# Performance work log

Measured on AMD Instinct MI355X. Metric: run time of the kernel, lower is better.

The kernel has to match this reference:

```python
import jax, jax.numpy as jnp
import numpy as np
from jax.ops import segment_sum, segment_max

ALPHA = 0.01  # leaky relu slope

def _cmul(a, b):
    # complex multiply on last-axis (re, im) pairs
    re = a[..., 0] * b[..., 0] - a[..., 1] * b[..., 1]
    im = a[..., 0] * b[..., 1] + a[..., 1] * b[..., 0]
    return jnp.stack((re, im), axis=-1)

def setup_inputs() -> dict:
    key = jax.random.key(0)
    ks = jax.random.split(key, 8)
    N, D, M, E, L, H, R, FH = 50000, 64, 3, 100000, 4, 8, 5, 128
    return {
        "features": jax.random.normal(ks[0], (N, D), jnp.float32),
        "attn1_w": jax.random.normal(ks[1], (M, H, D), jnp.float32) * 0.1,
        "attn2":   jax.random.normal(ks[2], (M, H, D), jnp.float32) * 0.1,
        "r_vec":   jax.random.normal(ks[3], (R, D // 2, 2), jnp.float32),
        "proj_w1": jax.random.normal(ks[4], (FH, H * D), jnp.float32) * 0.05,
        "proj_b1": jnp.zeros((FH,), jnp.float32),
        "proj_w2": jax.random.normal(ks[5], (1, FH), jnp.float32) * 0.1,
        "inst":    jax.random.randint(ks[6], (M, E, L), 0, N),
        "etypes":  jax.random.randint(ks[7], (M, L - 1), 0, 2 * R, dtype=jnp.int32),
    }

def reference(features, attn1_w, attn2, r_vec, proj_w1, proj_b1, proj_w2, inst, etypes):
    N, D = features.shape
    M, E, L = inst.shape
    H = attn1_w.shape[1]
    # --- conjugate-augmented, L2-normalized relation rotations ([2R, D/2, 2]) ---
    rn = r_vec / jnp.linalg.norm(r_vec, axis=2, keepdims=True)
    conj = rn * jnp.array([1.0, -1.0], rn.dtype)
    r_full = jnp.stack((rn, conj), axis=1).reshape(2 * r_vec.shape[0], r_vec.shape[1], 2)

    node_embs = []  # per-metapath [N, H*D]
    for m in range(M):
        # SemanticEncoder: gather + rotation recurrence + mean over path positions
        edata = features[inst[m]]                       # [E, L, D]
        edc = edata.reshape(E, L, D // 2, 2)
        # final_r_vec: backward cumulative complex product; position L-1 = identity
        ident = jnp.concatenate(
            [jnp.ones((D // 2, 1), edata.dtype), jnp.zeros((D // 2, 1), edata.dtype)], axis=-1)
        fr = [None] * L
        fr[L - 1] = ident
        for i in range(L - 2, -1, -1):
            fr[i] = _cmul(fr[i + 1], r_full[etypes[m, i]])
        fr = jnp.stack(fr, axis=0)                      # [L, D/2, 2]
        rotated = _cmul(edc, fr[None])                  # [E, L, D/2, 2] (pos L-1 rotated by identity)
        me = rotated.reshape(E, L, D).mean(axis=1)      # metapath embedding [E, D]

        # MessageAggregator: GAT-style segment softmax over instances per dst node
        dst = inst[m, :, 0]                             # [E]
        a1 = features[dst] @ attn1_w[m].T               # [E, H]
        a2 = jnp.einsum('ed,hd->eh', me, attn2[m])      # [E, H]
        a = jax.nn.leaky_relu(a1 + a2, ALPHA)           # [E, H]
        amax = segment_max(a, dst, num_segments=N)      # [N, H]
        amax = jnp.where(jnp.isfinite(amax), amax, 0.0)
        ex = jnp.exp(a - amax[dst])                     # [E, H]
        den = segment_sum(ex, dst, num_segments=N)      # [N, H]
        attn = ex / jnp.where(den[dst] > 0, den[dst], 1.0)
        agg = segment_sum(attn[:, :, None] * me[:, None, :], dst, num_segments=N)  # [N, H, D]
        node_embs.append(jax.nn.elu(agg).reshape(N, H * D))

    # Subgraph_Fusion: semantic attention over metapaths
    z = jnp.stack(node_embs, axis=1)                    # [N, M, H*D]
    w = jnp.tanh(z @ proj_w1.T + proj_b1) @ proj_w2.T   # [N, M, 1]
    beta = jax.nn.softmax(w.mean(axis=0), axis=0)       # [M, 1]
    out = (beta[None] * z).sum(axis=1)                  # [N, H*D]
    return out
```

## Files before the change

### kernel.cpp

```cpp
#include <hip/hip_runtime.h>
#include <hip/hip_bf16.h>
#include <hip/hip_fp16.h>
#include <math.h>

#define NN 50000
#define DD 64
#define MM 3
#define EE 100000
#define LL 4
#define HH 8
#define FHH 128
#define HD 512
#define NROWS (NN*MM)
#define LRELU_ALPHA 0.01f

#define WSUM_BINS 256
#define WSUM_SZ (MM*WSUM_BINS)
#define BINS (MM*NN)
#define NBLK ((BINS + 1023)/1024)
#define GT_TILE 224

#define FCVT_B 3125
#define CW1_B  64
#define UGEN_B 3
#define HISTG  392
#define HIST_B (HISTG*MM)
#define PREP_B (FCVT_B + CW1_B + UGEN_B + HIST_B + 1)

#define GT_B   (224*MM)
#define MID_B  (GT_B + NBLK)

#define SCAT_B (HISTG*MM)
#define SEGC_B ((BINS + 255)/256)
#define SCT_B  (SCAT_B + SEGC_B)

#define OFF_ZB    0
#define OFF_WSUM  (NROWS*HD/2)
#define OFF_BETA  (OFF_WSUM + WSUM_SZ)
#define OFF_W1BF  (OFF_BETA + 16)
#define OFF_WU    (OFF_W1BF + 32768)
#define OFF_FRS   (OFF_WU + 6144)
#define OFF_GT    (OFF_FRS + 768)
#define OFF_INTS  (OFF_GT + MM*NN*32)
#define IOFF_CNT    0
#define IOFF_CURSOR (IOFF_CNT + BINS)
#define IOFF_PART   (IOFF_CURSOR + BINS)
#define IOFF_BSUM   (IOFF_PART + BINS)
#define IOFF_BTOP   (IOFF_BSUM + 256)
#define IOFF_SEG8   (IOFF_BTOP + 256)
#define IOFF_REC    (IOFF_SEG8 + 8*BINS)
#define INTS_END    (IOFF_REC + 4*MM*EE)
#define OFF_F16   (OFF_INTS + INTS_END)

typedef short v8s __attribute__((ext_vector_type(8)));
typedef float v4f __attribute__((ext_vector_type(4)));

__device__ __forceinline__ float elu_f(float x) {
    return x > 0.f ? x : (__expf(x) - 1.f);
}

__device__ __forceinline__ float tanh_fast(float x) {
    float e = __expf(2.f * x);
    return 1.f - 2.f / (e + 1.f);
}

__device__ __forceinline__ unsigned int pk_bf16x2(float x, float y) {
    float2 f2; f2.x = x; f2.y = y;
    __hip_bfloat162 h = __float22bfloat162_rn(f2);
    union { __hip_bfloat162 h; unsigned int u; } cv;
    cv.h = h;
    return cv.u;
}

__device__ __forceinline__ unsigned int pk_h2(float x, float y) {
    __half2 h = __floats2half2_rn(x, y);
    union { __half2 h; unsigned int u; } cv;
    cv.h = h;
    return cv.u;
}

__device__ __forceinline__ float bf_lo(unsigned int u) {
    union { unsigned int x; float f; } c; c.x = u << 16; return c.f;
}
__device__ __forceinline__ float bf_hi(unsigned int u) {
    union { unsigned int x; float f; } c; c.x = u & 0xffff0000u; return c.f;
}

__device__ __forceinline__ __half2 u2h(unsigned int u) {
    union { unsigned int x; __half2 h; } c; c.x = u; return c.h;
}
__device__ __forceinline__ unsigned int h2u(__half2 h) {
    union { __half2 h; unsigned int x; } c; c.h = h; return c.x;
}

__device__ __forceinline__ unsigned int pk_fma(unsigned int x, unsigned int c, unsigned int a) {
    unsigned int d;
    asm("v_pk_fma_f16 %0, %1, %2, %3"
        : "=v"(d) : "v"(x), "v"(c), "v"(a));
    return d;
}
__device__ __forceinline__ unsigned int pk_fma_swap0(unsigned int x, unsigned int c, unsigned int a) {
    unsigned int d;
    asm("v_pk_fma_f16 %0, %1, %2, %3 op_sel:[1,0,0] op_sel_hi:[0,1,1]"
        : "=v"(d) : "v"(x), "v"(c), "v"(a));
    return d;
}
__device__ __forceinline__ unsigned int pk_fma_bcast0(unsigned int x, unsigned int c, unsigned int a) {
    unsigned int d;
    asm("v_pk_fma_f16 %0, %1, %2, %3 op_sel:[0,0,0] op_sel_hi:[0,1,1]"
        : "=v"(d) : "v"(x), "v"(c), "v"(a));
    return d;
}
__device__ __forceinline__ unsigned int pk_fma_bcast0hi(unsigned int x, unsigned int c, unsigned int a) {
    unsigned int d;
    asm("v_pk_fma_f16 %0, %1, %2, %3 op_sel:[1,0,0] op_sel_hi:[1,1,1]"
        : "=v"(d) : "v"(x), "v"(c), "v"(a));
    return d;
}

__device__ __forceinline__ void build_frs(
    float frs[LL][DD/2][2], const float* r_vec, const int* etypes, int m, int t)
{
    if (t < DD/2) {
        float cr = 1.f, ci = 0.f;
        frs[LL-1][t][0] = 1.f; frs[LL-1][t][1] = 0.f;
        for (int i = LL-2; i >= 0; --i) {
            int et = etypes[m*(LL-1) + i];
            float rr = r_vec[((et>>1)*(DD/2) + t)*2 + 0];
            float ri = r_vec[((et>>1)*(DD/2) + t)*2 + 1];
            float inv = rsqrtf(rr*rr + ri*ri);
            rr *= inv; ri *= inv;
            if (et & 1) ri = -ri;
            float nr = cr*rr - ci*ri;
            float ni = cr*ri + ci*rr;
            cr = nr; ci = ni;
            frs[i][t][0] = cr; frs[i][t][1] = ci;
        }
    }
}

__global__ __launch_bounds__(256) void prep_kernel(
    const float* __restrict__ features, ushort* __restrict__ f16,
    const float* __restrict__ w1, ushort* __restrict__ w1bf,
    const float* __restrict__ r_vec, const int* __restrict__ etypes,
    const float* __restrict__ attn1_w, const float* __restrict__ attn2,
    float* __restrict__ Wu, unsigned int* __restrict__ frs_h,
    const int* __restrict__ inst, int* __restrict__ cnt,
    float* __restrict__ wsum)
{
    const int b = blockIdx.x;
    const int t = threadIdx.x;
    if (b < FCVT_B) {
        int i = b*256 + t;
        float4 v = ((const float4*)features)[i];
        ((uint2*)f16)[i] = make_uint2(pk_h2(v.x, v.y), pk_h2(v.z, v.w));
    } else if (b < FCVT_B + CW1_B) {
        int i = (b - FCVT_B)*256 + t;
        float4 v = ((const float4*)w1)[i];
        uint2 p; p.x = pk_bf16x2(v.x, v.y); p.y = pk_bf16x2(v.z, v.w);
        ((uint2*)w1bf)[i] = p;
    } else if (b < FCVT_B + CW1_B + UGEN_B) {
        const int m = b - (FCVT_B + CW1_B);
        __shared__ float frs[LL][DD/2][2];
        build_frs(frs, r_vec, etypes, m, t);
        __syncthreads();
        if (t < 32) {
            unsigned int vals[8];
            #pragma unroll
            for (int l = 0; l < LL; ++l) {
                float fr = 0.25f * frs[l][t][0];
                float fi = 0.25f * frs[l][t][1];
                vals[2*l+0] = pk_h2(fr, fr);
                vals[2*l+1] = pk_h2(-fi, fi);
            }
            uint4* dst = (uint4*)frs_h + (m*32 + t)*2;
            dst[0] = make_uint4(vals[0], vals[1], vals[2], vals[3]);
            dst[1] = make_uint4(vals[4], vals[5], vals[6], vals[7]);
        }
        for (int idx = t; idx < 32*64; idx += 256) {
            int j = idx >> 6, d = idx & 63, p = d >> 1;
            int l = (j < 8) ? 0 : (j >> 3);
            int h = j & 7;
            float fr = frs[l][p][0], fi = frs[l][p][1];
            float w2r = attn2[m*HD + h*DD + 2*p];
            float w2i = attn2[m*HD + h*DD + 2*p + 1];
            float u = (d & 1) ? (fr*w2i - fi*w2r) : (fr*w2r + fi*w2i);
            float val = 0.25f * u + ((j < 8) ? attn1_w[m*HD + h*DD + d] : 0.f);
            Wu[(m*32 + j)*64 + d] = val;
        }
    } else if (b < FCVT_B + CW1_B + UGEN_B + HIST_B) {
        int idx = b - (FCVT_B + CW1_B + UGEN_B);
        int m = idx / HISTG;
        int e = (idx - m*HISTG)*256 + t;
        if (e < EE) {
            int dst = inst[((size_t)m*EE + e)*LL];
            atomicAdd(&cnt[m*NN + dst], 1);
        }
    } else {
        for (int i = t; i < WSUM_SZ; i += 256) wsum[i] = 0.f;
    }
}

__global__ __launch_bounds__(256) void mid_kernel(
    const float* __restrict__ features,
    const float* __restrict__ Wu,
    ushort* __restrict__ gt16,
    const int* __restrict__ cnt,
    int* __restrict__ part, int* __restrict__ bsum)
{
    __shared__ float xs[GT_TILE*65];
    __shared__ int sd[256];
    const int b = blockIdx.x;
    const int t = threadIdx.x;
    if (b < GT_B) {
        const int m = b / 224;
        const int node0 = (b - m*224) * GT_TILE;
        #pragma unroll
        for (int i = 0; i < 14; ++i) {
            int idx = t + 256*i;
            int r = idx >> 4, c4 = idx & 15;
            int gr = node0 + r;
            float4 v = make_float4(0.f,0.f,0.f,0.f);
            if (gr < NN) v = ((const float4*)features)[gr*16 + c4];
            float* dst = &xs[r*65 + c4*4];
            dst[0]=v.x; dst[1]=v.y; dst[2]=v.z; dst[3]=v.w;
        }
        __syncthreads();
        if (t >= GT_TILE) return;
        int node = node0 + t;
        float acc[32];
        #pragma unroll
        for (int j=0;j<32;++j) acc[j]=0.f;
        const float* Wm = Wu + m*2048;
        for (int d = 0; d < 64; ++d) {
            float x = xs[t*65 + d];
            #pragma unroll
            for (int j = 0; j < 32; ++j)
                acc[j] += x * Wm[j*64 + d];
        }
        if (node < NN) {
            ushort* o = gt16 + ((size_t)m*NN + node)*32;
            #pragma unroll
            for (int j4 = 0; j4 < 8; ++j4) {
                uint2 p;
                p.x = pk_h2(acc[j4*4+0], acc[j4*4+1]);
                p.y = pk_h2(acc[j4*4+2], acc[j4*4+3]);
                ((uint2*)o)[j4] = p;
            }
        }
    } else {
        const int bb = b - GT_B;
        const int base = bb*1024 + t*4;
        int v0=0,v1=0,v2=0,v3=0;
        if (base+3 < BINS) {
            int4 v = *(const int4*)&cnt[base];
            v0=v.x; v1=v.y; v2=v.z; v3=v.w;
        } else {
            if (base+0 < BINS) v0 = cnt[base+0];
            if (base+1 < BINS) v1 = cnt[base+1];
            if (base+2 < BINS) v2 = cnt[base+2];
            if (base+3 < BINS) v3 = cnt[base+3];
        }
        int tot = v0+v1+v2+v3;
        sd[t] = tot; __syncthreads();
        #pragma unroll
        for (int off = 1; off < 256; off <<= 1) {
            int val = (t >= off) ? sd[t-off] : 0;
            __syncthreads();
            sd[t] += val;
            __syncthreads();
        }
        int excl = sd[t] - tot;
        if (base+0 < BINS) part[base+0] = excl;
        if (base+1 < BINS) part[base+1] = excl + v0;
        if (base+2 < BINS) part[base+2] = excl + v0 + v1;
        if (base+3 < BINS) part[base+3] = excl + v0 + v1 + v2;
        if (t == 255) bsum[bb] = sd[255];
    }
}

__global__ __launch_bounds__(256) void scan_tops_kernel(
    const int* __restrict__ bsum, int* __restrict__ btop)
{
    __shared__ int sd[256];
    const int t = threadIdx.x;
    int v = (t < NBLK) ? bsum[t] : 0;
    sd[t] = v; __syncthreads();
    #pragma unroll
    for (int off = 1; off < 256; off <<= 1) {
        int val = (t >= off) ? sd[t-off] : 0;
        __syncthreads();
        sd[t] += val;
        __syncthreads();
    }
    if (t < NBLK) btop[t] = sd[t] - v;
}

__global__ __launch_bounds__(256) void scat_kernel(
    const int4* __restrict__ inst4, const int* __restrict__ part,
    const int* __restrict__ btop, int* __restrict__ cursor,
    int4* __restrict__ rec, const int* __restrict__ cnt,
    int* __restrict__ seg8)
{
    const int b = blockIdx.x;
    const int t = threadIdx.x;
    if (b < SCAT_B) {
        int m = b / HISTG;
        int e = (b - m*HISTG)*256 + t;
        if (e >= EE) return;
        int4 v = inst4[(size_t)m*EE + e];
        int bin = m*NN + v.x;
        int c = atomicAdd(&cursor[bin], 1);
        int pos = part[bin] + btop[bin >> 10] + c;
        rec[pos] = make_int4(v.y, v.z, v.w, 0);
        if (c < 2) {
            int* s = seg8 + bin*8 + 2 + c*3;
            s[0] = v.y; s[1] = v.z; s[2] = v.w;
        }
    } else {
        int i = (b - SCAT_B)*256 + t;
        if (i < BINS)
            ((int2*)seg8)[i*4] = make_int2(part[i] + btop[i >> 10], cnt[i]);
    }
}

__global__ __launch_bounds__(128) void node_kernel(
    const unsigned int* __restrict__ f16u,
    const unsigned int* __restrict__ frs_h,
    const int4*  __restrict__ rec4,
    const int*   __restrict__ seg8,
    const ushort* __restrict__ gt16,
    ushort* __restrict__ Zb)
{
    const int m = blockIdx.y;
    const int t = threadIdx.x;
    const int lane = t & 63;
    const int hl   = lane & 31;
    const int half = lane >> 5;
    const int wid  = t >> 6;
    const int node = blockIdx.x*2 + wid;

    const int bin = m*NN + node;
    ushort* zrow = Zb + ((size_t)node*MM + m)*HD;
    const int4 sa = ((const int4*)seg8)[bin*2 + 0];
    const int4 sb = ((const int4*)seg8)[bin*2 + 1];

    const uint4* fh = (const uint4*)frs_h + ((size_t)(m*32 + hl))*2;
    const uint4 ca = fh[0], cb = fh[1];
    const unsigned int ux0 = f16u[(size_t)node*32 + hl];
    const float c0 = __half2float(((const __half*)gt16)[(size_t)bin*32 + (hl & 7)]);

    const int start = __builtin_amdgcn_readfirstlane(sa.x);
    const int ecnt  = __builtin_amdgcn_readfirstlane(sa.y);
    if (ecnt == 0) {
        ((uint4*)zrow)[lane] = make_uint4(0u,0u,0u,0u);
        return;
    }

    int4 rpre = make_int4(0,0,0,0);
    if (ecnt > 2) {
        int myq = 2 + half;
        int qq = (myq < ecnt) ? myq : (ecnt - 1);
        rpre = rec4[start + qq];
    }

    unsigned int me0u = h2u(__hmul2(u2h(ux0), u2h(ca.x)));
    me0u = pk_fma_swap0(ux0, ca.y, me0u);

    const int lsel = hl >> 3;
    const bool gm = (hl >= 8);
    const __half* gtmh = (const __half*)gt16 + (size_t)m*NN*32;

    unsigned int acc[HH];
    #pragma unroll
    for (int h = 0; h < HH; ++h) acc[h] = 0u;
    float den = 0.f;

    auto edge = [&](int i1, int i2, int i3, bool valid) {
        int idxg = (lsel == 1) ? i1 : ((lsel == 2) ? i2 : i3);
        float gv = 0.f;
        if (gm) gv = __half2float(gtmh[(size_t)idxg*32 + hl]);
        unsigned int u1 = f16u[(size_t)i1*32 + hl];
        unsigned int u2 = f16u[(size_t)i2*32 + hl];
        unsigned int u3 = f16u[(size_t)i3*32 + hl];
        gv += __shfl_xor(gv, 16);
        gv += __shfl_xor(gv, 8);
        unsigned int me = me0u;
        me = pk_fma(u1, ca.z, me);
        me = pk_fma_swap0(u1, ca.w, me);
        me = pk_fma(u2, cb.x, me);
        me = pk_fma_swap0(u2, cb.y, me);
        me = pk_fma(u3, cb.z, me);
        me = pk_fma_swap0(u3, cb.w, me);
        float a = c0 + gv;
        a = fmaxf(a, LRELU_ALPHA*a);
        float ex = valid ? __expf(a) : 0.f;
        den += ex;
        float exn = __shfl_xor(ex, 1);
        unsigned int ex2 = pk_h2(ex, exn);
        #pragma unroll
        for (int j = 0; j < 4; ++j) {
            unsigned int eu = __shfl(ex2, (lane & 32) + 2*j);
            acc[2*j]   = pk_fma_bcast0  (eu, me, acc[2*j]);
            acc[2*j+1] = pk_fma_bcast0hi(eu, me, acc[2*j+1]);
        }
    };

    {
        bool useB = (half == 1) && (ecnt >= 2);
        int i1 = useB ? sb.y : sa.z;
        int i2 = useB ? sb.z : sa.w;
        int i3 = useB ? sb.w : sb.x;
        edge(i1, i2, i3, half == 0 || ecnt >= 2);
    }
    if (ecnt > 2) {
        edge(rpre.x, rpre.y, rpre.z, (2 + half) < ecnt);
        for (int q = 4; q < ecnt; q += 2) {
            int myq = q + half;
            bool valid = (myq < ecnt);
            int qq = valid ? myq : (ecnt - 1);
            int4 r = rec4[start + qq];
            edge(r.x, r.y, r.z, valid);
        }
    }

    #pragma unroll
    for (int h = 0; h < HH; ++h) {
        unsigned int au = __shfl_xor(acc[h], 32);
        acc[h] = h2u(__hadd2(u2h(acc[h]), u2h(au)));
    }
    den += __shfl_xor(den, 32);

    const int hbase = half ? 4 : 0;
    #pragma unroll
    for (int hh = 0; hh < 4; ++hh) {
        int h = hbase + hh;
        unsigned int sel = half ? acc[hh+4] : acc[hh];
        float dh = __shfl(den, h);
        float inv = __builtin_amdgcn_rcpf(dh);
        float2 v = __half22float2(u2h(sel));
        float vr = elu_f(v.x * inv);
        float vi = elu_f(v.y * inv);
        ((unsigned int*)zrow)[h*32 + hl] = pk_bf16x2(vr, vi);
    }
}


__global__ __launch_bounds__(256,3) void wproj_kernel(
    const ushort* __restrict__ Zb,
    const ushort* __restrict__ w1bf,
    const float* __restrict__ b1,
    const float* __restrict__ w2,
    float* __restrict__ wsum)
{
    __shared__ ushort As[128*72];
    __shared__ ushort Bs[128*72];
    __shared__ float wacc[MM];
    const int t = threadIdx.x;
    const int row0 = blockIdx.x * 128;
    if (t < MM) wacc[t] = 0.f;
    const int lane = t & 63;
    const int wid  = t >> 6;
    const int ln   = lane & 15;
    const int quad = lane >> 4;
    const int wr   = wid >> 1;
    const int wc   = wid & 1;

    v4f acc[4][4];
    #pragma unroll
    for (int i=0;i<4;++i)
        #pragma unroll
        for (int j=0;j<4;++j)
            acc[i][j] = (v4f){0.f,0.f,0.f,0.f};

    const uint4* zb4 = (const uint4*)Zb;
    const uint4* wb4 = (const uint4*)w1bf;

    for (int kt = 0; kt < 8; ++kt) {
        __syncthreads();
        #pragma unroll
        for (int i = 0; i < 4; ++i) {
            int idx = t + 256*i;
            int r = idx >> 3, k8 = idx & 7;
            int gr = row0 + r;
            uint4 v = make_uint4(0u,0u,0u,0u);
            if (gr < NROWS) v = zb4[(size_t)gr*64 + kt*8 + k8];
            *(uint4*)&As[r*72 + k8*8] = v;
        }
        #pragma unroll
        for (int i = 0; i < 4; ++i) {
            int idx = t + 256*i;
            int f = idx >> 3, k8 = idx & 7;
            uint4 v = wb4[f*64 + kt*8 + k8];
            *(uint4*)&Bs[f*72 + k8*8] = v;
        }
        __syncthreads();
        #pragma unroll
        for (int kk = 0; kk < 2; ++kk) {
            v8s a[4], b[4];
            #pragma unroll
            for (int i=0;i<4;++i)
                a[i] = *(const v8s*)&As[(wr*64 + i*16 + ln)*72 + kk*32 + quad*8];
            #pragma unroll
            for (int j=0;j<4;++j)
                b[j] = *(const v8s*)&Bs[(wc*64 + j*16 + ln)*72 + kk*32 + quad*8];
            #pragma unroll
            for (int i=0;i<4;++i)
                #pragma unroll
                for (int j=0;j<4;++j)
                    acc[i][j] = __builtin_amdgcn_mfma_f32_16x16x32_bf16(
                        a[i], b[j], acc[i][j], 0, 0, 0);
        }
    }

    float b1v[4], w2v[4];
    #pragma unroll
    for (int j=0;j<4;++j) {
        int col = wc*64 + j*16 + ln;
        b1v[j] = b1[col];
        w2v[j] = w2[col];
    }
    #pragma unroll
    for (int i=0;i<4;++i) {
        #pragma unroll
        for (int reg=0;reg<4;++reg) {
            float s = 0.f;
            #pragma unroll
            for (int j=0;j<4;++j)
                s += tanh_fast(acc[i][j][reg] + b1v[j]) * w2v[j];
            s += __shfl_xor(s, 1);
            s += __shfl_xor(s, 2);
            s += __shfl_xor(s, 4);
            s += __shfl_xor(s, 8);
            int grow = row0 + wr*64 + i*16 + quad*4 + reg;
            if (ln == 0 && grow < NROWS)
                atomicAdd(&wacc[grow % MM], s);
        }
    }
    __syncthreads();
    if (t < MM)
        atomicAdd(&wsum[t*WSUM_BINS + (blockIdx.x & (WSUM_BINS-1))], wacc[t]);
}

__global__ void beta_kernel(const float* __restrict__ wsum, float* __restrict__ beta)
{
    __shared__ float sm[MM];
    int t = threadIdx.x;
    if (t < MM) {
        float s = 0.f;
        for (int i = 0; i < WSUM_BINS; ++i) s += wsum[t*WSUM_BINS + i];
        sm[t] = s / (float)NN;
    }
    __syncthreads();
    if (t < MM) {
        float a = sm[0], b = sm[1], c = sm[2];
        float mx = fmaxf(a, fmaxf(b, c));
        float e0 = __expf(a-mx), e1 = __expf(b-mx), e2 = __expf(c-mx);
        float tot = e0+e1+e2;
        float mine = (t==0?e0:(t==1?e1:e2));
        beta[t] = mine/tot;
    }
}

__global__ __launch_bounds__(256) void out_kernel(
    const ushort* __restrict__ Zb, const float* __restrict__ beta,
    float* __restrict__ out)
{
    int i = blockIdx.x*256 + threadIdx.x;
    int n  = i >> 6;
    int jj = i & 63;
    float b0 = beta[0], b1v = beta[1], b2 = beta[2];
    const uint4* zb4 = (const uint4*)Zb;
    uint4 v0 = zb4[((size_t)n*MM + 0)*64 + jj];
    uint4 v1 = zb4[((size_t)n*MM + 1)*64 + jj];
    uint4 v2 = zb4[((size_t)n*MM + 2)*64 + jj];
    float o[8];
    o[0] = b0*bf_lo(v0.x) + b1v*bf_lo(v1.x) + b2*bf_lo(v2.x);
    o[1] = b0*bf_hi(v0.x) + b1v*bf_hi(v1.x) + b2*bf_hi(v2.x);
    o[2] = b0*bf_lo(v0.y) + b1v*bf_lo(v1.y) + b2*bf_lo(v2.y);
    o[3] = b0*bf_hi(v0.y) + b1v*bf_hi(v1.y) + b2*bf_hi(v2.y);
    o[4] = b0*bf_lo(v0.z) + b1v*bf_lo(v1.z) + b2*bf_lo(v2.z);
    o[5] = b0*bf_hi(v0.z) + b1v*bf_hi(v1.z) + b2*bf_hi(v2.z);
    o[6] = b0*bf_lo(v0.w) + b1v*bf_lo(v1.w) + b2*bf_lo(v2.w);
    o[7] = b0*bf_hi(v0.w) + b1v*bf_hi(v1.w) + b2*bf_hi(v2.w);
    float4* op = (float4*)(out + (size_t)n*HD + jj*8);
    op[0] = make_float4(o[0],o[1],o[2],o[3]);
    op[1] = make_float4(o[4],o[5],o[6],o[7]);
}

extern "C" void kernel_launch(void* const* d_in, const int* in_sizes, int n_in,
                              void* d_out, int out_size, void* d_ws, size_t ws_size,
                              hipStream_t stream) {
    const float* features = (const float*)d_in[0];
    const float* attn1_w  = (const float*)d_in[1];
    const float* attn2    = (const float*)d_in[2];
    const float* r_vec    = (const float*)d_in[3];
    const float* proj_w1  = (const float*)d_in[4];
    const float* proj_b1  = (const float*)d_in[5];
    const float* proj_w2  = (const float*)d_in[6];
    const int*   inst     = (const int*)d_in[7];
    const int*   etypes   = (const int*)d_in[8];
    float* out = (float*)d_out;

    float* ws    = (float*)d_ws;
    ushort* Zb   = (ushort*)(ws + OFF_ZB);
    float* wsum  = ws + OFF_WSUM;
    float* beta  = ws + OFF_BETA;
    ushort* w1bf = (ushort*)(ws + OFF_W1BF);
    float* Wu    = ws + OFF_WU;
    unsigned int* frs_h = (unsigned int*)(ws + OFF_FRS);
    ushort* gt16 = (ushort*)(ws + OFF_GT);
    int* ints    = (int*)(ws + OFF_INTS);
    int* cnt     = ints + IOFF_CNT;
    int* cursor  = ints + IOFF_CURSOR;
    int* part    = ints + IOFF_PART;
    int* bsum    = ints + IOFF_BSUM;
    int* btop    = ints + IOFF_BTOP;
    int* seg8    = ints + IOFF_SEG8;
    int4* rec4   = (int4*)(ints + IOFF_REC);
    ushort* f16  = (ushort*)(ws + OFF_F16);

    hipMemsetAsync(cnt, 0, (size_t)2*BINS*sizeof(int), stream);

    prep_kernel<<<PREP_B, 256, 0, stream>>>(
        features, f16, proj_w1, w1bf, r_vec, etypes, attn1_w, attn2,
        Wu, frs_h, inst, cnt, wsum);
    mid_kernel<<<MID_B, 256, 0, stream>>>(features, Wu, gt16, cnt, part, bsum);
    scan_tops_kernel<<<1, 256, 0, stream>>>(bsum, btop);
    scat_kernel<<<SCT_B, 256, 0, stream>>>(
        (const int4*)inst, part, btop, cursor, rec4, cnt, seg8);
    node_kernel<<<dim3(NN/2, MM), 128, 0, stream>>>(
        (const unsigned int*)f16, frs_h, rec4, seg8, gt16, Zb);
    wproj_kernel<<<(NROWS + 127)/128, 256, 0, stream>>>(Zb, w1bf, proj_b1, proj_w2, wsum);
    beta_kernel<<<1, 64, 0, stream>>>(wsum, beta);
    out_kernel<<<NN*64/256, 256, 0, stream>>>(Zb, beta, out);
}
```

Measured before the change: 353.2 us.

## Map one node per half-wavefront in node_kernel instead of one per wavefront

Each half-wave of 32 lanes now owns a separate destination node and walks that node's edges serially, so a 64-lane wave handles two nodes. Before, the two halves split one node's edges and then merged their results with cross-half shuffles. The change removes the cross-half reduction and halves the grid, with the aim of cutting idle lanes when a node has few edges. In exchange, the loop runs to the larger of the two nodes' edge counts, so one half-wave idles through padded iterations when counts differ. It also adds a guard for a zero denominator.

Measured after the change: 344.6 us. 1.02x faster.

```diff
diff --git a/kernel.cpp b/kernel.cpp
--- a/kernel.cpp
+++ b/kernel.cpp
@@ -338,7 +338,7 @@
     const int hl   = lane & 31;
     const int half = lane >> 5;
     const int wid  = t >> 6;
-    const int node = blockIdx.x*2 + wid;
+    const int node = blockIdx.x*4 + wid*2 + half;
 
     const int bin = m*NN + node;
     ushort* zrow = Zb + ((size_t)node*MM + m)*HD;
@@ -350,18 +350,14 @@
     const unsigned int ux0 = f16u[(size_t)node*32 + hl];
     const float c0 = __half2float(((const __half*)gt16)[(size_t)bin*32 + (hl & 7)]);
 
-    const int start = __builtin_amdgcn_readfirstlane(sa.x);
-    const int ecnt  = __builtin_amdgcn_readfirstlane(sa.y);
-    if (ecnt == 0) {
-        ((uint4*)zrow)[lane] = make_uint4(0u,0u,0u,0u);
+    const int start = sa.x;
+    const int ecnt  = sa.y;
+    int eo = __shfl_xor(ecnt, 32);
+    int emax = __builtin_amdgcn_readfirstlane(max(ecnt, eo));
+    if (emax == 0) {
+        ((uint4*)zrow)[hl] = make_uint4(0u,0u,0u,0u);
+        ((uint4*)zrow)[hl + 32] = make_uint4(0u,0u,0u,0u);
         return;
-    }
-
-    int4 rpre = make_int4(0,0,0,0);
-    if (ecnt > 2) {
-        int myq = 2 + half;
-        int qq = (myq < ecnt) ? myq : (ecnt - 1);
-        rpre = rec4[start + qq];
     }
 
     unsigned int me0u = h2u(__hmul2(u2h(ux0), u2h(ca.x)));
@@ -376,7 +372,18 @@
     for (int h = 0; h < HH; ++h) acc[h] = 0u;
     float den = 0.f;
 
-    auto edge = [&](int i1, int i2, int i3, bool valid) {
+    for (int q = 0; q < emax; ++q) {
+        bool valid = (q < ecnt);
+        int i1, i2, i3;
+        if (q == 0)      { i1 = sa.z; i2 = sa.w; i3 = sb.x; }
+        else if (q == 1) { i1 = sb.y; i2 = sb.z; i3 = sb.w; }
+        else {
+            int qq = valid ? q : (ecnt > 0 ? ecnt - 1 : 0);
+            int4 r = rec4[start + qq];
+            i1 = r.x; i2 = r.y; i3 = r.z;
+        }
+        if (!valid) { i1 = node; i2 = node; i3 = node; }
+
         int idxg = (lsel == 1) ? i1 : ((lsel == 2) ? i2 : i3);
         float gv = 0.f;
         if (gm) gv = __half2float(gtmh[(size_t)idxg*32 + hl]);
@@ -404,41 +411,13 @@
             acc[2*j]   = pk_fma_bcast0  (eu, me, acc[2*j]);
             acc[2*j+1] = pk_fma_bcast0hi(eu, me, acc[2*j+1]);
         }
-    };
-
-    {
-        bool useB = (half == 1) && (ecnt >= 2);
-        int i1 = useB ? sb.y : sa.z;
-        int i2 = useB ? sb.z : sa.w;
-        int i3 = useB ? sb.w : sb.x;
-        edge(i1, i2, i3, half == 0 || ecnt >= 2);
-    }
-    if (ecnt > 2) {
-        edge(rpre.x, rpre.y, rpre.z, (2 + half) < ecnt);
-        for (int q = 4; q < ecnt; q += 2) {
-            int myq = q + half;
-            bool valid = (myq < ecnt);
-            int qq = valid ? myq : (ecnt - 1);
-            int4 r = rec4[start + qq];
-            edge(r.x, r.y, r.z, valid);
-        }
     }
 
     #pragma unroll
     for (int h = 0; h < HH; ++h) {
-        unsigned int au = __shfl_xor(acc[h], 32);
-        acc[h] = h2u(__hadd2(u2h(acc[h]), u2h(au)));
-    }
-    den += __shfl_xor(den, 32);
-
-    const int hbase = half ? 4 : 0;
-    #pragma unroll
-    for (int hh = 0; hh < 4; ++hh) {
-        int h = hbase + hh;
-        unsigned int sel = half ? acc[hh+4] : acc[hh];
-        float dh = __shfl(den, h);
-        float inv = __builtin_amdgcn_rcpf(dh);
-        float2 v = __half22float2(u2h(sel));
+        float dh = __shfl(den, (lane & 32) + h);
+        float inv = (dh > 0.f) ? __builtin_amdgcn_rcpf(dh) : 0.f;
+        float2 v = __half22float2(u2h(acc[h]));
         float vr = elu_f(v.x * inv);
         float vi = elu_f(v.y * inv);
         ((unsigned int*)zrow)[h*32 + hl] = pk_bf16x2(vr, vi);
@@ -629,7 +608,7 @@
     scan_tops_kernel<<<1, 256, 0, stream>>>(bsum, btop);
     scat_kernel<<<SCT_B, 256, 0, stream>>>(
         (const int4*)inst, part, btop, cursor, rec4, cnt, seg8);
-    node_kernel<<<dim3(NN/2, MM), 128, 0, stream>>>(
+    node_kernel<<<dim3(NN/4, MM), 128, 0, stream>>>(
         (const unsigned int*)f16, frs_h, rec4, seg8, gt16, Zb);
     wproj_kernel<<<(NROWS + 127)/128, 256, 0, stream>>>(Zb, w1bf, proj_b1, proj_w2, wsum);
     beta_kernel<<<1, 64, 0, stream>>>(wsum, beta);
```
